# Optimization experiments

Hardware: AMD Instinct MI355X
Metric: run time of the kernel (lower is better)

## Reference

```python
import jax, jax.numpy as jnp
import numpy as np

N = 50000
E = 800000
IN = 128
HEADS = 4
C = 32  # out_features per head
HC = HEADS * C


def setup_inputs() -> dict:
    key = jax.random.key(0)
    ks = jax.random.split(key, 10)
    s_in = 1.0 / np.sqrt(IN)
    x = jax.random.normal(ks[0], (N, IN), dtype=jnp.float32)
    edge_index = jax.random.randint(ks[1], (2, E), 0, N, dtype=jnp.int64)
    Wq = jax.random.normal(ks[2], (IN, HC), dtype=jnp.float32) * s_in
    bq = jnp.zeros((HC,), dtype=jnp.float32)
    Wk = jax.random.normal(ks[3], (IN, HC), dtype=jnp.float32) * s_in
    bk = jnp.zeros((HC,), dtype=jnp.float32)
    Wv = jax.random.normal(ks[4], (IN, HC), dtype=jnp.float32) * s_in
    bv = jnp.zeros((HC,), dtype=jnp.float32)
    Wskip = jax.random.normal(ks[5], (IN, HC), dtype=jnp.float32) * s_in
    bskip = jnp.zeros((HC,), dtype=jnp.float32)
    return {"x": x, "edge_index": edge_index, "Wq": Wq, "bq": bq,
            "Wk": Wk, "bk": bk, "Wv": Wv, "bv": bv,
            "Wskip": Wskip, "bskip": bskip}


def reference(x, edge_index, Wq, bq, Wk, bk, Wv, bv, Wskip, bskip):
    src = edge_index[0]  # message source j
    dst = edge_index[1]  # message target i

    q = (x @ Wq + bq).reshape(N, HEADS, C)
    k = (x @ Wk + bk).reshape(N, HEADS, C)
    v = (x @ Wv + bv).reshape(N, HEADS, C)

    # per-edge attention logits: [E, H]
    logits = jnp.einsum('ehc,ehc->eh', q[dst], k[src]) / jnp.sqrt(
        jnp.asarray(C, dtype=x.dtype))

    # segment softmax over incoming edges of each target node
    seg_max = jax.ops.segment_max(logits, dst, num_segments=N)
    seg_max = jnp.where(jnp.isfinite(seg_max), seg_max, 0.0)
    expd = jnp.exp(logits - seg_max[dst])
    seg_sum = jax.ops.segment_sum(expd, dst, num_segments=N)
    alpha = expd / (seg_sum[dst] + 1e-16)  # [E, H]

    # scatter-add weighted values: [N, H, C]
    msgs = alpha[:, :, None] * v[src]
    out = jax.ops.segment_sum(msgs, dst, num_segments=N)
    out = out.reshape(N, HC) + (x @ Wskip + bskip)  # root/skip connection

    # LeakyReLU(negative_slope=0.2)
    return jnp.where(out >= 0, out, 0.2 * out)
```

## Files before the change

kernel.cpp:

```cpp
#include <hip/hip_runtime.h>

#define N_NODES 50000
#define E_EDGES 800000
#define IN_F 128
#define HC 128
#define NCOLS 512
#define ROWTILES 3125
#define SCAN_BLOCKS 196

typedef __attribute__((ext_vector_type(8))) short short8;
typedef __attribute__((ext_vector_type(4))) float floatx4;

__device__ __forceinline__ unsigned short f2bf(float f) {
    union { float f; unsigned u; } x; x.f = f;
    unsigned r = x.u + 0x7FFF + ((x.u >> 16) & 1);
    return (unsigned short)(r >> 16);
}

__global__ __launch_bounds__(256) void pack_w(
    const float* __restrict__ Wq, const float* __restrict__ Wk,
    const float* __restrict__ Wv, const float* __restrict__ Ws,
    const float* __restrict__ bq, const float* __restrict__ bk,
    const float* __restrict__ bv, const float* __restrict__ bs,
    short* __restrict__ bpack, float* __restrict__ bcat)
{
    int t = blockIdx.x * 256 + threadIdx.x;
    int lane = t & 63, ks = (t >> 6) & 3, nt = t >> 8;
    int col = nt * 16 + (lane & 15);
    int sec = col >> 7, c = col & 127;
    const float* W = sec == 0 ? Wq : sec == 1 ? Wk : sec == 2 ? Wv : Ws;
    int kbase = ks * 32 + (lane >> 4) * 8;
    short8 b;
#pragma unroll
    for (int j = 0; j < 8; j++) b[j] = (short)f2bf(W[(size_t)(kbase + j) * HC + c]);
    *(short8*)(bpack + (size_t)t * 8) = b;
    if (t < NCOLS) {
        int s2 = t >> 7, c2 = t & 127;
        bcat[t] = (s2 == 0 ? bq : s2 == 1 ? bk : s2 == 2 ? bv : bs)[c2];
    }
}

__global__ __launch_bounds__(256) void gemm_mfma(
    const float* __restrict__ x, const short* __restrict__ bpack,
    const float* __restrict__ bcat,
    unsigned short* __restrict__ q, unsigned short* __restrict__ k,
    unsigned short* __restrict__ v, float* __restrict__ out)
{
    const int rt = blockIdx.x;
    const int cg = threadIdx.x >> 6;
    const int lane = threadIdx.x & 63;
    const int m0 = rt * 16 + (lane & 15);
    const int koff = (lane >> 4) * 8;

    short8 a0[4];
#pragma unroll
    for (int ks = 0; ks < 4; ks++) {
        const float* p0 = x + (size_t)m0 * IN_F + ks * 32 + koff;
        float4 lo = *(const float4*)p0;
        float4 hi = *(const float4*)(p0 + 4);
        short8 a;
        a[0] = (short)f2bf(lo.x); a[1] = (short)f2bf(lo.y);
        a[2] = (short)f2bf(lo.z); a[3] = (short)f2bf(lo.w);
        a[4] = (short)f2bf(hi.x); a[5] = (short)f2bf(hi.y);
        a[6] = (short)f2bf(hi.z); a[7] = (short)f2bf(hi.w);
        a0[ks] = a;
    }

    unsigned short* dstb = (cg == 0) ? q : (cg == 1) ? k : v;
    const int rb0 = rt * 16 + (lane >> 4) * 4;

#pragma unroll
    for (int nt8 = 0; nt8 < 8; nt8++) {
        const int nt = cg * 8 + nt8;
        floatx4 acc = {0.f, 0.f, 0.f, 0.f};
#pragma unroll
        for (int ks = 0; ks < 4; ks++) {
            short8 b = *(const short8*)(bpack + ((size_t)(nt * 4 + ks) * 64 + lane) * 8);
            acc = __builtin_amdgcn_mfma_f32_16x16x32_bf16(a0[ks], b, acc, 0, 0, 0);
        }
        const int c = nt8 * 16 + (lane & 15);
        const float bias = bcat[cg * 128 + c];
        if (cg < 3) {
#pragma unroll
            for (int r = 0; r < 4; r++)
                dstb[(size_t)(rb0 + r) * HC + c] = f2bf(acc[r] + bias);
        } else {
#pragma unroll
            for (int r = 0; r < 4; r++)
                out[(size_t)(rb0 + r) * HC + c] = acc[r] + bias;
        }
    }
}

__global__ __launch_bounds__(256) void hist_k(const int* __restrict__ dst,
                                              int* __restrict__ cnt,
                                              int* __restrict__ rank)
{
    int e = blockIdx.x * 256 + threadIdx.x;
    if (e < E_EDGES) rank[e] = atomicAdd(&cnt[dst[e]], 1);
}

__device__ __forceinline__ int block_incl_scan(int val, int t, int* wsum) {
    const int lane = t & 63, w = t >> 6;
    int incl = val;
#pragma unroll
    for (int off = 1; off < 64; off <<= 1) {
        int u = __shfl_up(incl, off);
        if (lane >= off) incl += u;
    }
    if (lane == 63) wsum[w] = incl;
    __syncthreads();
    int pre = 0;
#pragma unroll
    for (int i = 0; i < 4; i++) if (i < w) pre += wsum[i];
    return incl + pre;
}

__global__ __launch_bounds__(256) void bsum_k(const int* __restrict__ cnt,
                                              int* __restrict__ bsum)
{
    __shared__ int wsum[4];
    int idx = blockIdx.x * 256 + threadIdx.x;
    int val = (idx < N_NODES) ? cnt[idx] : 0;
    const int lane = threadIdx.x & 63, w = threadIdx.x >> 6;
    int s = val;
#pragma unroll
    for (int off = 32; off >= 1; off >>= 1) s += __shfl_xor(s, off);
    if (lane == 0) wsum[w] = s;
    __syncthreads();
    if (threadIdx.x == 0)
        bsum[blockIdx.x] = wsum[0] + wsum[1] + wsum[2] + wsum[3];
}

__global__ __launch_bounds__(256) void bscan_k(const int* __restrict__ bsum,
                                               int* __restrict__ boff)
{
    __shared__ int wsum[4];
    const int t = threadIdx.x;
    int val = (t < SCAN_BLOCKS) ? bsum[t] : 0;
    int incl = block_incl_scan(val, t, wsum);
    if (t < SCAN_BLOCKS) boff[t] = incl - val;
}

__global__ __launch_bounds__(256) void bapply_k(const int* __restrict__ cnt,
                                                const int* __restrict__ boff,
                                                int* __restrict__ rowptr)
{
    __shared__ int wsum[4];
    int idx = blockIdx.x * 256 + threadIdx.x;
    int val = (idx < N_NODES) ? cnt[idx] : 0;
    int incl = block_incl_scan(val, threadIdx.x, wsum);
    int excl = boff[blockIdx.x] + incl - val;
    if (idx < N_NODES) rowptr[idx] = excl;
    if (idx == N_NODES - 1) rowptr[N_NODES] = E_EDGES;
}

__global__ __launch_bounds__(256) void scatter_k(const int* __restrict__ src,
                                                 const int* __restrict__ dst,
                                                 const int* __restrict__ rowptr,
                                                 const int* __restrict__ rank,
                                                 int* __restrict__ ssrc)
{
    int e = blockIdx.x * 256 + threadIdx.x;
    if (e < E_EDGES) ssrc[rowptr[dst[e]] + rank[e]] = src[e];
}

__global__ __launch_bounds__(256) void node_attn(
    const unsigned short* __restrict__ q, const unsigned short* __restrict__ k,
    const unsigned short* __restrict__ v, const int* __restrict__ rowptr,
    const int* __restrict__ ssrc, float* __restrict__ out)
{
    const int wave = (blockIdx.x * 256 + threadIdx.x) >> 6;
    if (wave >= N_NODES) return;
    const int lane = threadIdx.x & 63;
    const int node = wave;

    union { unsigned u; float f; } cv;
    const unsigned uq = *(const unsigned*)(q + (size_t)node * HC + lane * 2);
    cv.u = uq << 16;          float qx = cv.f;
    cv.u = uq & 0xFFFF0000u;  float qy = cv.f;

    float accx = 0.f, accy = 0.f, ssum = 0.f;
    const int beg = __builtin_amdgcn_readfirstlane(rowptr[node]);
    const int end = __builtin_amdgcn_readfirstlane(rowptr[node + 1]);
    const float scale = 0.17677669529663687f;

    int e = beg;
    for (; e + 3 < end; e += 4) {
        const int j0 = ssrc[e],     j1 = ssrc[e + 1];
        const int j2 = ssrc[e + 2], j3 = ssrc[e + 3];
        const unsigned uk0 = *(const unsigned*)(k + (size_t)j0 * HC + lane * 2);
        const unsigned uk1 = *(const unsigned*)(k + (size_t)j1 * HC + lane * 2);
        const unsigned uk2 = *(const unsigned*)(k + (size_t)j2 * HC + lane * 2);
        const unsigned uk3 = *(const unsigned*)(k + (size_t)j3 * HC + lane * 2);
        const unsigned uv0 = *(const unsigned*)(v + (size_t)j0 * HC + lane * 2);
        const unsigned uv1 = *(const unsigned*)(v + (size_t)j1 * HC + lane * 2);
        const unsigned uv2 = *(const unsigned*)(v + (size_t)j2 * HC + lane * 2);
        const unsigned uv3 = *(const unsigned*)(v + (size_t)j3 * HC + lane * 2);
        float p0, p1, p2, p3;
        { float kx, ky;
          cv.u = uk0 << 16; kx = cv.f; cv.u = uk0 & 0xFFFF0000u; ky = cv.f;
          p0 = qx * kx + qy * ky;
          cv.u = uk1 << 16; kx = cv.f; cv.u = uk1 & 0xFFFF0000u; ky = cv.f;
          p1 = qx * kx + qy * ky;
          cv.u = uk2 << 16; kx = cv.f; cv.u = uk2 & 0xFFFF0000u; ky = cv.f;
          p2 = qx * kx + qy * ky;
          cv.u = uk3 << 16; kx = cv.f; cv.u = uk3 & 0xFFFF0000u; ky = cv.f;
          p3 = qx * kx + qy * ky; }
#pragma unroll
        for (int off = 1; off <= 8; off <<= 1) {
            p0 += __shfl_xor(p0, off);
            p1 += __shfl_xor(p1, off);
            p2 += __shfl_xor(p2, off);
            p3 += __shfl_xor(p3, off);
        }
        const float w0 = __expf(p0 * scale);
        const float w1 = __expf(p1 * scale);
        const float w2 = __expf(p2 * scale);
        const float w3 = __expf(p3 * scale);
        { float vx, vy;
          cv.u = uv0 << 16; vx = cv.f; cv.u = uv0 & 0xFFFF0000u; vy = cv.f;
          accx += w0 * vx; accy += w0 * vy;
          cv.u = uv1 << 16; vx = cv.f; cv.u = uv1 & 0xFFFF0000u; vy = cv.f;
          accx += w1 * vx; accy += w1 * vy;
          cv.u = uv2 << 16; vx = cv.f; cv.u = uv2 & 0xFFFF0000u; vy = cv.f;
          accx += w2 * vx; accy += w2 * vy;
          cv.u = uv3 << 16; vx = cv.f; cv.u = uv3 & 0xFFFF0000u; vy = cv.f;
          accx += w3 * vx; accy += w3 * vy; }
        ssum += (w0 + w1) + (w2 + w3);
    }
    for (; e < end; e++) {
        const int j0 = ssrc[e];
        const unsigned uk0 = *(const unsigned*)(k + (size_t)j0 * HC + lane * 2);
        const unsigned uv0 = *(const unsigned*)(v + (size_t)j0 * HC + lane * 2);
        float kx, ky;
        cv.u = uk0 << 16; kx = cv.f; cv.u = uk0 & 0xFFFF0000u; ky = cv.f;
        float p0 = qx * kx + qy * ky;
        p0 += __shfl_xor(p0, 1);
        p0 += __shfl_xor(p0, 2);
        p0 += __shfl_xor(p0, 4);
        p0 += __shfl_xor(p0, 8);
        const float w0 = __expf(p0 * scale);
        float vx, vy;
        cv.u = uv0 << 16; vx = cv.f; cv.u = uv0 & 0xFFFF0000u; vy = cv.f;
        accx += w0 * vx; accy += w0 * vy;
        ssum += w0;
    }

    const float inv = 1.0f / (ssum + 1e-16f);
    const float2 sk = *(const float2*)(out + (size_t)node * HC + lane * 2);
    float ox = accx * inv + sk.x;
    float oy = accy * inv + sk.y;
    ox = ox >= 0.f ? ox : 0.2f * ox;
    oy = oy >= 0.f ? oy : 0.2f * oy;
    *(float2*)(out + (size_t)node * HC + lane * 2) = make_float2(ox, oy);
}

extern "C" void kernel_launch(void* const* d_in, const int* in_sizes, int n_in,
                              void* d_out, int out_size, void* d_ws, size_t ws_size,
                              hipStream_t stream)
{
    const float* x    = (const float*)d_in[0];
    const int*   ei   = (const int*)d_in[1];
    const float* Wq   = (const float*)d_in[2];
    const float* bq   = (const float*)d_in[3];
    const float* Wk   = (const float*)d_in[4];
    const float* bk   = (const float*)d_in[5];
    const float* Wv   = (const float*)d_in[6];
    const float* bv   = (const float*)d_in[7];
    const float* Wsk  = (const float*)d_in[8];
    const float* bsk  = (const float*)d_in[9];
    float* out = (float*)d_out;

    char* w = (char*)d_ws;
    const size_t NFB = (size_t)N_NODES * HC * sizeof(unsigned short);
    unsigned short* q = (unsigned short*)w;            w += NFB;
    unsigned short* k = (unsigned short*)w;            w += NFB;
    unsigned short* v = (unsigned short*)w;            w += NFB;
    short* bpack = (short*)w;                          w += 8192 * 8 * sizeof(short);
    float* bcat  = (float*)w;                          w += NCOLS * sizeof(float);
    int* cnt    = (int*)w;                             w += N_NODES * sizeof(int);
    int* rowptr = (int*)w;                             w += (N_NODES + 1) * sizeof(int);
    int* bsum   = (int*)w;                             w += SCAN_BLOCKS * sizeof(int);
    int* boff   = (int*)w;                             w += SCAN_BLOCKS * sizeof(int);
    int* rank   = (int*)w;                             w += (size_t)E_EDGES * sizeof(int);
    int* ssrc   = (int*)w;

    const int* srcIdx = ei;
    const int* dstIdx = ei + E_EDGES;

    hipMemsetAsync(cnt, 0, N_NODES * sizeof(int), stream);

    pack_w<<<32, 256, 0, stream>>>(Wq, Wk, Wv, Wsk, bq, bk, bv, bsk, bpack, bcat);
    hist_k<<<(E_EDGES + 255) / 256, 256, 0, stream>>>(dstIdx, cnt, rank);
    gemm_mfma<<<ROWTILES, 256, 0, stream>>>(x, bpack, bcat, q, k, v, out);
    bsum_k<<<SCAN_BLOCKS, 256, 0, stream>>>(cnt, bsum);
    bscan_k<<<1, 256, 0, stream>>>(bsum, boff);
    bapply_k<<<SCAN_BLOCKS, 256, 0, stream>>>(cnt, boff, rowptr);
    scatter_k<<<(E_EDGES + 255) / 256, 256, 0, stream>>>(srcIdx, dstIdx, rowptr, rank, ssrc);
    node_attn<<<(N_NODES * 64) / 256, 256, 0, stream>>>(q, k, v, rowptr, ssrc, out);
}
```

Baseline: 161.0 us.

## Fuse pack/hist and scan kernels; process four edges per wave in node attention

```diff
diff --git a/kernel.cpp b/kernel.cpp
--- a/kernel.cpp
+++ b/kernel.cpp
@@ -7,6 +7,8 @@
 #define NCOLS 512
 #define ROWTILES 3125
 #define SCAN_BLOCKS 196
+#define PACK_BLOCKS 32
+#define HIST_BLOCKS ((E_EDGES + 255) / 256)
 
 typedef __attribute__((ext_vector_type(8))) short short8;
 typedef __attribute__((ext_vector_type(4))) float floatx4;
@@ -16,27 +18,39 @@
     unsigned r = x.u + 0x7FFF + ((x.u >> 16) & 1);
     return (unsigned short)(r >> 16);
 }
-
-__global__ __launch_bounds__(256) void pack_w(
+__device__ __forceinline__ float bflo(unsigned u) {
+    union { unsigned u; float f; } c; c.u = u << 16; return c.f;
+}
+__device__ __forceinline__ float bfhi(unsigned u) {
+    union { unsigned u; float f; } c; c.u = u & 0xFFFF0000u; return c.f;
+}
+
+__global__ __launch_bounds__(256) void pack_hist_k(
     const float* __restrict__ Wq, const float* __restrict__ Wk,
     const float* __restrict__ Wv, const float* __restrict__ Ws,
     const float* __restrict__ bq, const float* __restrict__ bk,
     const float* __restrict__ bv, const float* __restrict__ bs,
-    short* __restrict__ bpack, float* __restrict__ bcat)
-{
-    int t = blockIdx.x * 256 + threadIdx.x;
-    int lane = t & 63, ks = (t >> 6) & 3, nt = t >> 8;
-    int col = nt * 16 + (lane & 15);
-    int sec = col >> 7, c = col & 127;
-    const float* W = sec == 0 ? Wq : sec == 1 ? Wk : sec == 2 ? Wv : Ws;
-    int kbase = ks * 32 + (lane >> 4) * 8;
-    short8 b;
-#pragma unroll
-    for (int j = 0; j < 8; j++) b[j] = (short)f2bf(W[(size_t)(kbase + j) * HC + c]);
-    *(short8*)(bpack + (size_t)t * 8) = b;
-    if (t < NCOLS) {
-        int s2 = t >> 7, c2 = t & 127;
-        bcat[t] = (s2 == 0 ? bq : s2 == 1 ? bk : s2 == 2 ? bv : bs)[c2];
+    short* __restrict__ bpack, float* __restrict__ bcat,
+    const int* __restrict__ dst, int* __restrict__ cnt, int* __restrict__ rank)
+{
+    if (blockIdx.x < PACK_BLOCKS) {
+        int t = blockIdx.x * 256 + threadIdx.x;
+        int lane = t & 63, ks = (t >> 6) & 3, nt = t >> 8;
+        int col = nt * 16 + (lane & 15);
+        int sec = col >> 7, c = col & 127;
+        const float* W = sec == 0 ? Wq : sec == 1 ? Wk : sec == 2 ? Wv : Ws;
+        int kbase = ks * 32 + (lane >> 4) * 8;
+        short8 b;
+#pragma unroll
+        for (int j = 0; j < 8; j++) b[j] = (short)f2bf(W[(size_t)(kbase + j) * HC + c]);
+        *(short8*)(bpack + (size_t)t * 8) = b;
+        if (t < NCOLS) {
+            int s2 = t >> 7, c2 = t & 127;
+            bcat[t] = (s2 == 0 ? bq : s2 == 1 ? bk : s2 == 2 ? bv : bs)[c2];
+        }
+    } else {
+        int e = (blockIdx.x - PACK_BLOCKS) * 256 + threadIdx.x;
+        if (e < E_EDGES) rank[e] = atomicAdd(&cnt[dst[e]], 1);
     }
 }
 
@@ -92,16 +106,25 @@
     }
 }
 
-__global__ __launch_bounds__(256) void hist_k(const int* __restrict__ dst,
-                                              int* __restrict__ cnt,
-                                              int* __restrict__ rank)
-{
-    int e = blockIdx.x * 256 + threadIdx.x;
-    if (e < E_EDGES) rank[e] = atomicAdd(&cnt[dst[e]], 1);
-}
-
-__device__ __forceinline__ int block_incl_scan(int val, int t, int* wsum) {
+__global__ __launch_bounds__(256) void scan_apply(const int* __restrict__ cnt,
+                                                  int* __restrict__ rowptr)
+{
+    __shared__ int wsum[4];
+    const int t = threadIdx.x;
     const int lane = t & 63, w = t >> 6;
+    const int limit = blockIdx.x * 256;
+
+    int s = 0;
+    for (int i = t; i < limit; i += 256) s += cnt[i];
+#pragma unroll
+    for (int off = 32; off >= 1; off >>= 1) s += __shfl_xor(s, off);
+    if (lane == 0) wsum[w] = s;
+    __syncthreads();
+    const int prefix = wsum[0] + wsum[1] + wsum[2] + wsum[3];
+    __syncthreads();
+
+    int idx = limit + t;
+    int val = (idx < N_NODES) ? cnt[idx] : 0;
     int incl = val;
 #pragma unroll
     for (int off = 1; off < 64; off <<= 1) {
@@ -113,44 +136,7 @@
     int pre = 0;
 #pragma unroll
     for (int i = 0; i < 4; i++) if (i < w) pre += wsum[i];
-    return incl + pre;
-}
-
-__global__ __launch_bounds__(256) void bsum_k(const int* __restrict__ cnt,
-                                              int* __restrict__ bsum)
-{
-    __shared__ int wsum[4];
-    int idx = blockIdx.x * 256 + threadIdx.x;
-    int val = (idx < N_NODES) ? cnt[idx] : 0;
-    const int lane = threadIdx.x & 63, w = threadIdx.x >> 6;
-    int s = val;
-#pragma unroll
-    for (int off = 32; off >= 1; off >>= 1) s += __shfl_xor(s, off);
-    if (lane == 0) wsum[w] = s;
-    __syncthreads();
-    if (threadIdx.x == 0)
-        bsum[blockIdx.x] = wsum[0] + wsum[1] + wsum[2] + wsum[3];
-}
-
-__global__ __launch_bounds__(256) void bscan_k(const int* __restrict__ bsum,
-                                               int* __restrict__ boff)
-{
-    __shared__ int wsum[4];
-    const int t = threadIdx.x;
-    int val = (t < SCAN_BLOCKS) ? bsum[t] : 0;
-    int incl = block_incl_scan(val, t, wsum);
-    if (t < SCAN_BLOCKS) boff[t] = incl - val;
-}
-
-__global__ __launch_bounds__(256) void bapply_k(const int* __restrict__ cnt,
-                                                const int* __restrict__ boff,
-                                                int* __restrict__ rowptr)
-{
-    __shared__ int wsum[4];
-    int idx = blockIdx.x * 256 + threadIdx.x;
-    int val = (idx < N_NODES) ? cnt[idx] : 0;
-    int incl = block_incl_scan(val, threadIdx.x, wsum);
-    int excl = boff[blockIdx.x] + incl - val;
+    int excl = prefix + pre + incl - val;
     if (idx < N_NODES) rowptr[idx] = excl;
     if (idx == N_NODES - 1) rowptr[N_NODES] = E_EDGES;
 }
@@ -174,86 +160,71 @@
     if (wave >= N_NODES) return;
     const int lane = threadIdx.x & 63;
     const int node = wave;
-
-    union { unsigned u; float f; } cv;
-    const unsigned uq = *(const unsigned*)(q + (size_t)node * HC + lane * 2);
-    cv.u = uq << 16;          float qx = cv.f;
-    cv.u = uq & 0xFFFF0000u;  float qy = cv.f;
-
-    float accx = 0.f, accy = 0.f, ssum = 0.f;
+    const int g = lane >> 4;
+    const int l16 = lane & 15;
+    const int c0 = l16 * 8;
+
+    const uint4 uq = *(const uint4*)(q + (size_t)node * HC + c0);
+    float qf[8];
+    qf[0] = bflo(uq.x); qf[1] = bfhi(uq.x);
+    qf[2] = bflo(uq.y); qf[3] = bfhi(uq.y);
+    qf[4] = bflo(uq.z); qf[5] = bfhi(uq.z);
+    qf[6] = bflo(uq.w); qf[7] = bfhi(uq.w);
+
+    float acc[8];
+#pragma unroll
+    for (int i = 0; i < 8; i++) acc[i] = 0.f;
+    float ssum = 0.f;
+
     const int beg = __builtin_amdgcn_readfirstlane(rowptr[node]);
     const int end = __builtin_amdgcn_readfirstlane(rowptr[node + 1]);
     const float scale = 0.17677669529663687f;
 
-    int e = beg;
-    for (; e + 3 < end; e += 4) {
-        const int j0 = ssrc[e],     j1 = ssrc[e + 1];
-        const int j2 = ssrc[e + 2], j3 = ssrc[e + 3];
-        const unsigned uk0 = *(const unsigned*)(k + (size_t)j0 * HC + lane * 2);
-        const unsigned uk1 = *(const unsigned*)(k + (size_t)j1 * HC + lane * 2);
-        const unsigned uk2 = *(const unsigned*)(k + (size_t)j2 * HC + lane * 2);
-        const unsigned uk3 = *(const unsigned*)(k + (size_t)j3 * HC + lane * 2);
-        const unsigned uv0 = *(const unsigned*)(v + (size_t)j0 * HC + lane * 2);
-        const unsigned uv1 = *(const unsigned*)(v + (size_t)j1 * HC + lane * 2);
-        const unsigned uv2 = *(const unsigned*)(v + (size_t)j2 * HC + lane * 2);
-        const unsigned uv3 = *(const unsigned*)(v + (size_t)j3 * HC + lane * 2);
-        float p0, p1, p2, p3;
-        { float kx, ky;
-          cv.u = uk0 << 16; kx = cv.f; cv.u = uk0 & 0xFFFF0000u; ky = cv.f;
-          p0 = qx * kx + qy * ky;
-          cv.u = uk1 << 16; kx = cv.f; cv.u = uk1 & 0xFFFF0000u; ky = cv.f;
-          p1 = qx * kx + qy * ky;
-          cv.u = uk2 << 16; kx = cv.f; cv.u = uk2 & 0xFFFF0000u; ky = cv.f;
-          p2 = qx * kx + qy * ky;
-          cv.u = uk3 << 16; kx = cv.f; cv.u = uk3 & 0xFFFF0000u; ky = cv.f;
-          p3 = qx * kx + qy * ky; }
-#pragma unroll
-        for (int off = 1; off <= 8; off <<= 1) {
-            p0 += __shfl_xor(p0, off);
-            p1 += __shfl_xor(p1, off);
-            p2 += __shfl_xor(p2, off);
-            p3 += __shfl_xor(p3, off);
-        }
-        const float w0 = __expf(p0 * scale);
-        const float w1 = __expf(p1 * scale);
-        const float w2 = __expf(p2 * scale);
-        const float w3 = __expf(p3 * scale);
-        { float vx, vy;
-          cv.u = uv0 << 16; vx = cv.f; cv.u = uv0 & 0xFFFF0000u; vy = cv.f;
-          accx += w0 * vx; accy += w0 * vy;
-          cv.u = uv1 << 16; vx = cv.f; cv.u = uv1 & 0xFFFF0000u; vy = cv.f;
-          accx += w1 * vx; accy += w1 * vy;
-          cv.u = uv2 << 16; vx = cv.f; cv.u = uv2 & 0xFFFF0000u; vy = cv.f;
-          accx += w2 * vx; accy += w2 * vy;
-          cv.u = uv3 << 16; vx = cv.f; cv.u = uv3 & 0xFFFF0000u; vy = cv.f;
-          accx += w3 * vx; accy += w3 * vy; }
-        ssum += (w0 + w1) + (w2 + w3);
-    }
-    for (; e < end; e++) {
-        const int j0 = ssrc[e];
-        const unsigned uk0 = *(const unsigned*)(k + (size_t)j0 * HC + lane * 2);
-        const unsigned uv0 = *(const unsigned*)(v + (size_t)j0 * HC + lane * 2);
-        float kx, ky;
-        cv.u = uk0 << 16; kx = cv.f; cv.u = uk0 & 0xFFFF0000u; ky = cv.f;
-        float p0 = qx * kx + qy * ky;
-        p0 += __shfl_xor(p0, 1);
-        p0 += __shfl_xor(p0, 2);
-        p0 += __shfl_xor(p0, 4);
-        p0 += __shfl_xor(p0, 8);
-        const float w0 = __expf(p0 * scale);
-        float vx, vy;
-        cv.u = uv0 << 16; vx = cv.f; cv.u = uv0 & 0xFFFF0000u; vy = cv.f;
-        accx += w0 * vx; accy += w0 * vy;
-        ssum += w0;
-    }
-
-    const float inv = 1.0f / (ssum + 1e-16f);
-    const float2 sk = *(const float2*)(out + (size_t)node * HC + lane * 2);
-    float ox = accx * inv + sk.x;
-    float oy = accy * inv + sk.y;
-    ox = ox >= 0.f ? ox : 0.2f * ox;
-    oy = oy >= 0.f ? oy : 0.2f * oy;
-    *(float2*)(out + (size_t)node * HC + lane * 2) = make_float2(ox, oy);
+    for (int e = beg; e < end; e += 4) {
+        const int ee = e + g;
+        const int jj = ssrc[ee < end ? ee : beg];
+        const uint4 uk = *(const uint4*)(k + (size_t)jj * HC + c0);
+        const uint4 uv = *(const uint4*)(v + (size_t)jj * HC + c0);
+
+        float p = qf[0] * bflo(uk.x) + qf[1] * bfhi(uk.x)
+                + qf[2] * bflo(uk.y) + qf[3] * bfhi(uk.y)
+                + qf[4] * bflo(uk.z) + qf[5] * bfhi(uk.z)
+                + qf[6] * bflo(uk.w) + qf[7] * bfhi(uk.w);
+        p += __shfl_xor(p, 1);
+        p += __shfl_xor(p, 2);
+        float wgt = __expf(p * scale);
+        wgt = (ee < end) ? wgt : 0.f;
+        ssum += wgt;
+
+        acc[0] += wgt * bflo(uv.x); acc[1] += wgt * bfhi(uv.x);
+        acc[2] += wgt * bflo(uv.y); acc[3] += wgt * bfhi(uv.y);
+        acc[4] += wgt * bflo(uv.z); acc[5] += wgt * bfhi(uv.z);
+        acc[6] += wgt * bflo(uv.w); acc[7] += wgt * bfhi(uv.w);
+    }
+
+    ssum += __shfl_xor(ssum, 16);
+    ssum += __shfl_xor(ssum, 32);
+#pragma unroll
+    for (int i = 0; i < 8; i++) {
+        acc[i] += __shfl_xor(acc[i], 16);
+        acc[i] += __shfl_xor(acc[i], 32);
+    }
+
+    if (g == 0) {
+        const float inv = 1.0f / (ssum + 1e-16f);
+        float* op = out + (size_t)node * HC + c0;
+        float4 s0 = *(const float4*)op;
+        float4 s1 = *(const float4*)(op + 4);
+        float o[8];
+        o[0] = acc[0] * inv + s0.x; o[1] = acc[1] * inv + s0.y;
+        o[2] = acc[2] * inv + s0.z; o[3] = acc[3] * inv + s0.w;
+        o[4] = acc[4] * inv + s1.x; o[5] = acc[5] * inv + s1.y;
+        o[6] = acc[6] * inv + s1.z; o[7] = acc[7] * inv + s1.w;
+#pragma unroll
+        for (int i = 0; i < 8; i++) o[i] = o[i] >= 0.f ? o[i] : 0.2f * o[i];
+        *(float4*)op       = make_float4(o[0], o[1], o[2], o[3]);
+        *(float4*)(op + 4) = make_float4(o[4], o[5], o[6], o[7]);
+    }
 }
 
 extern "C" void kernel_launch(void* const* d_in, const int* in_sizes, int n_in,
@@ -281,8 +252,6 @@
     float* bcat  = (float*)w;                          w += NCOLS * sizeof(float);
     int* cnt    = (int*)w;                             w += N_NODES * sizeof(int);
     int* rowptr = (int*)w;                             w += (N_NODES + 1) * sizeof(int);
-    int* bsum   = (int*)w;                             w += SCAN_BLOCKS * sizeof(int);
-    int* boff   = (int*)w;                             w += SCAN_BLOCKS * sizeof(int);
     int* rank   = (int*)w;                             w += (size_t)E_EDGES * sizeof(int);
     int* ssrc   = (int*)w;
 
@@ -291,12 +260,10 @@
 
     hipMemsetAsync(cnt, 0, N_NODES * sizeof(int), stream);
 
-    pack_w<<<32, 256, 0, stream>>>(Wq, Wk, Wv, Wsk, bq, bk, bv, bsk, bpack, bcat);
-    hist_k<<<(E_EDGES + 255) / 256, 256, 0, stream>>>(dstIdx, cnt, rank);
+    pack_hist_k<<<PACK_BLOCKS + HIST_BLOCKS, 256, 0, stream>>>(
+        Wq, Wk, Wv, Wsk, bq, bk, bv, bsk, bpack, bcat, dstIdx, cnt, rank);
     gemm_mfma<<<ROWTILES, 256, 0, stream>>>(x, bpack, bcat, q, k, v, out);
-    bsum_k<<<SCAN_BLOCKS, 256, 0, stream>>>(cnt, bsum);
-    bscan_k<<<1, 256, 0, stream>>>(bsum, boff);
-    bapply_k<<<SCAN_BLOCKS, 256, 0, stream>>>(cnt, boff, rowptr);
+    scan_apply<<<SCAN_BLOCKS, 256, 0, stream>>>(cnt, rowptr);
     scatter_k<<<(E_EDGES + 255) / 256, 256, 0, stream>>>(srcIdx, dstIdx, rowptr, rank, ssrc);
     node_attn<<<(N_NODES * 64) / 256, 256, 0, stream>>>(q, k, v, rowptr, ssrc, out);
 }
```

Measured after the change: 181.3 us. 1.13x slower.
